# Kernel tuning notes

Measured on AMD Instinct MI355X. Metric: run time of the kernel, lower is better.

## Reference

```python
import jax, jax.numpy as jnp
import numpy as np

B, Q, K = 8, 128, 1024
QK_DIM = 512   # query_size == key_size
HID = 256      # hidden_size
VDIM = 512     # value feature dim
NEG = -1e6     # mask fill value used by the torch code


def setup_inputs() -> dict:
    key = jax.random.key(0)
    ks = jax.random.split(key, 7)
    queries = jax.random.normal(ks[0], (B, Q, QK_DIM), dtype=jnp.float32)
    keys = jax.random.normal(ks[1], (B, K, QK_DIM), dtype=jnp.float32)
    values = jax.random.normal(ks[2], (B, K, VDIM), dtype=jnp.float32)
    valid_lens = jax.random.randint(ks[3], (B,), 1, K + 1, dtype=jnp.int32)
    # Linear weights (no bias); scaled like torch default init
    Wq = jax.random.normal(ks[4], (QK_DIM, HID), dtype=jnp.float32) / np.sqrt(QK_DIM)
    Wk = jax.random.normal(ks[5], (QK_DIM, HID), dtype=jnp.float32) / np.sqrt(QK_DIM)
    wv = jax.random.normal(ks[6], (HID,), dtype=jnp.float32) / np.sqrt(HID)
    return {"queries": queries, "keys": keys, "values": values,
            "valid_lens": valid_lens, "Wq": Wq, "Wk": Wk, "wv": wv}


def reference(queries, keys, values, valid_lens, Wq, Wk, wv):
    q = jnp.einsum('bqd,dh->bqh', queries, Wq)          # [B,Q,H]
    k = jnp.einsum('bkd,dh->bkh', keys, Wk)             # [B,K,H]
    # broadcast add -> tanh -> score projection
    features = jnp.tanh(q[:, :, None, :] + k[:, None, :, :])  # [B,Q,K,H]
    scores = jnp.einsum('bqkh,h->bqk', features, wv)    # [B,Q,K]
    # masked softmax over last axis (valid_lens per batch row)
    mask = jnp.arange(scores.shape[-1])[None, None, :] < valid_lens[:, None, None]
    scores = jnp.where(mask, scores, NEG)
    attn = jax.nn.softmax(scores, axis=-1)              # [B,Q,K]
    # dropout is identity in eval mode (p=0)
    return jnp.einsum('bqk,bkv->bqv', attn, values)     # [B,Q,VDIM]
```

## Files before the change

### kernel.cpp

```cpp
#include <hip/hip_runtime.h>
#include <math.h>

#define NB 8
#define NQ 128
#define NK 1024
#define ND 512
#define NH 256
#define NV 512

typedef __attribute__((ext_vector_type(8))) short short8v;
typedef __attribute__((ext_vector_type(4))) float floatx4;


__device__ __forceinline__ ushort f2bf(float f) {
  union { float f; unsigned u; } v; v.f = f;
  unsigned r = (v.u + 0x7FFF + ((v.u >> 16) & 1)) >> 16;
  return (ushort)r;
}
__device__ __forceinline__ float bf2f(ushort b) {
  union { unsigned u; float f; } v; v.u = ((unsigned)b) << 16;
  return v.f;
}
__device__ __forceinline__ float wave_rsum(float v) {
#pragma unroll
  for (int off = 32; off; off >>= 1) v += __shfl_xor(v, off);
  return v;
}

__global__ __launch_bounds__(64) void splitw_kernel(
    const float* __restrict__ Wq, const float* __restrict__ Wk,
    ushort* __restrict__ WpQ, ushort* __restrict__ WpK) {
  const int l = threadIdx.x;
  const int blk = blockIdx.x;
  const float* W = blockIdx.y ? Wk : Wq;
  ushort* O = blockIdx.y ? WpK : WpQ;
  const int col = ((blk >> 4) << 4) + (l & 15);
  const int dbase = (blk & 15) * 32 + ((l >> 4) << 3);
  ushort h8[8], l8[8];
#pragma unroll
  for (int j = 0; j < 8; ++j) {
    float f = W[(size_t)(dbase + j) * NH + col];
    ushort hi = f2bf(f);
    h8[j] = hi;
    l8[j] = f2bf(f - bf2f(hi));
  }
  ushort* oh = &O[(size_t)blk * 1024 + l * 8];
  *(ushort4*)&oh[0] = make_ushort4(h8[0], h8[1], h8[2], h8[3]);
  *(ushort4*)&oh[4] = make_ushort4(h8[4], h8[5], h8[6], h8[7]);
  *(ushort4*)&oh[512] = make_ushort4(l8[0], l8[1], l8[2], l8[3]);
  *(ushort4*)&oh[516] = make_ushort4(l8[4], l8[5], l8[6], l8[7]);
}

__global__ __launch_bounds__(256) void convert_v_kernel(
    const float* __restrict__ values, const int* __restrict__ valid_lens,
    ushort* __restrict__ Vp) {
  const int b = blockIdx.z;
  const int k0 = blockIdx.x * 32;
  const int v0 = blockIdx.y * 32;
  const int V = valid_lens[b];
  if (k0 >= ((V + 31) & ~31)) return;
  const int t = threadIdx.x;
  __shared__ float tile[32][33];
#pragma unroll
  for (int i = 0; i < 4; ++i) {
    int idx = t + 256 * i;
    int kk = idx >> 5, vv = idx & 31;
    tile[kk][vv] = values[(size_t)(b * NK + k0 + kk) * NV + v0 + vv];
  }
  __syncthreads();
  const int vv = t & 31, k4 = t >> 5;
  const int kr = k4 * 4;
  const size_t base = ((size_t)(b * 32 + ((v0 + vv) >> 4)) * 32 + (k0 >> 5)) * 512;
  const int off = ((vv & 15) << 3) + (((kr >> 3) & 3) << 7) + (kr & 7);
  ushort4 o;
  o.x = f2bf(tile[kr + 0][vv]);
  o.y = f2bf(tile[kr + 1][vv]);
  o.z = f2bf(tile[kr + 2][vv]);
  o.w = f2bf(tile[kr + 3][vv]);
  *(ushort4*)&Vp[base + off] = o;
}

__global__ __launch_bounds__(256, 2) void proj_mfma_kernel(
    const float* __restrict__ queries, const float* __restrict__ keys,
    const ushort* __restrict__ WpQ, const ushort* __restrict__ WpK,
    const int* __restrict__ valid_lens,
    float* __restrict__ Eq, ushort* __restrict__ EkTb) {
  const int t = threadIdx.x;
  const int lane = t & 63, wvid = t >> 6;
  const int lr = lane & 15, lg = lane >> 4;
  const int bx = blockIdx.x;
  const bool isQ = bx < 64;
  const float* A;
  const ushort* Wp;
  int arow0, b = 0, rin = 0;
  if (isQ) {
    A = queries; Wp = WpQ; arow0 = bx * 16;
  } else {
    int kt = bx - 64;
    b = kt >> 6; rin = (kt & 63) * 16;
    if (rin >= valid_lens[b]) return;
    A = keys; Wp = WpK; arow0 = b * NK + rin;
  }

  __shared__ ushort Ah[16][520];
  __shared__ ushort Al[16][520];
  {
    const float* Arow = A + (size_t)arow0 * ND;
#pragma unroll
    for (int i = 0; i < 8; ++i) {
      int e = (t + 256 * i) * 4;
      int r = e >> 9, c = e & 511;
      float4 a = *(const float4*)&Arow[e];
      ushort4 h, l;
      h.x = f2bf(a.x); l.x = f2bf(a.x - bf2f(h.x));
      h.y = f2bf(a.y); l.y = f2bf(a.y - bf2f(h.y));
      h.z = f2bf(a.z); l.z = f2bf(a.z - bf2f(h.z));
      h.w = f2bf(a.w); l.w = f2bf(a.w - bf2f(h.w));
      *(ushort4*)&Ah[r][c] = h;
      *(ushort4*)&Al[r][c] = l;
    }
  }
  __syncthreads();

  const ushort* wbase = Wp + (size_t)wvid * 64 * 1024 + lane * 8;

  floatx4 acc[4];
#pragma unroll
  for (int c = 0; c < 4; ++c) acc[c] = (floatx4){0.f, 0.f, 0.f, 0.f};

  short8v wh[3][4], wl[3][4];
  short8v ahb[2], alb[2];

#define LOADW(buf, kkv)                                                    \
  {                                                                        \
    _Pragma("unroll") for (int c = 0; c < 4; ++c) {                        \
      wh[buf][c] = *(const short8v*)&wbase[(size_t)(c * 16 + (kkv)) * 1024];        \
      wl[buf][c] = *(const short8v*)&wbase[(size_t)(c * 16 + (kkv)) * 1024 + 512];  \
    }                                                                      \
  }
#define LOADA(buf, kkv)                                                    \
  {                                                                        \
    ahb[buf] = *(const short8v*)&Ah[lr][(kkv) * 32 + lg * 8];              \
    alb[buf] = *(const short8v*)&Al[lr][(kkv) * 32 + lg * 8];              \
  }

  LOADW(0, 0);
  LOADW(1, 1);
  LOADA(0, 0);
#pragma unroll
  for (int kk = 0; kk < 16; ++kk) {
    if (kk + 2 < 16) LOADW((kk + 2) % 3, kk + 2);
    if (kk + 1 < 16) LOADA((kk + 1) & 1, kk + 1);
    const short8v ah_ = ahb[kk & 1];
    const short8v al_ = alb[kk & 1];
    const int B = kk % 3;
#pragma unroll
    for (int c = 0; c < 4; ++c) {
      acc[c] = __builtin_amdgcn_mfma_f32_16x16x32_bf16(al_, wh[B][c], acc[c], 0, 0, 0);
      acc[c] = __builtin_amdgcn_mfma_f32_16x16x32_bf16(ah_, wl[B][c], acc[c], 0, 0, 0);
      acc[c] = __builtin_amdgcn_mfma_f32_16x16x32_bf16(ah_, wh[B][c], acc[c], 0, 0, 0);
    }
  }
#undef LOADW
#undef LOADA

  const float C2 = 2.885390081777927f;
  if (isQ) {
#pragma unroll
    for (int c = 0; c < 4; ++c) {
      const int h = wvid * 64 + c * 16 + lr;
#pragma unroll
      for (int reg = 0; reg < 4; ++reg) {
        const int row = arow0 + lg * 4 + reg;
        float p = fminf(fmaxf(acc[c][reg], -15.f), 15.f);
        Eq[(size_t)row * NH + h] = exp2f(p * C2);
      }
    }
  } else {
#pragma unroll
    for (int c = 0; c < 4; ++c) {
      const int h = wvid * 64 + c * 16 + lr;
      ushort4 e;
      e.x = f2bf(exp2f(fminf(fmaxf(acc[c][0], -15.f), 15.f) * C2));
      e.y = f2bf(exp2f(fminf(fmaxf(acc[c][1], -15.f), 15.f) * C2));
      e.z = f2bf(exp2f(fminf(fmaxf(acc[c][2], -15.f), 15.f) * C2));
      e.w = f2bf(exp2f(fminf(fmaxf(acc[c][3], -15.f), 15.f) * C2));
      *(ushort4*)&EkTb[((size_t)(b * NH + h)) * NK + rin + lg * 4] = e;
    }
  }
}

__global__ __launch_bounds__(256, 2) void score_kernel(
    const float* __restrict__ Eq, const ushort* __restrict__ EkTb,
    const float* __restrict__ wvp, const int* __restrict__ valid_lens,
    ushort* __restrict__ Pbp, float* __restrict__ rowsum) {
  const int b = blockIdx.z;
  const int V = valid_lens[b];
  const int k0 = blockIdx.y * 256;
  if (k0 >= V) return;
  const int t = threadIdx.x;
  const int q0 = blockIdx.x * 2;
  const int lane = t & 63, wid = t >> 6;
  const float L2E2 = 2.8853900817779268f;

  __shared__ __align__(16) float eqs[2][NH];
  __shared__ __align__(16) float wvs[NH];
  __shared__ float red[8];

  if (t < 128)
    ((float4*)eqs)[t] = ((const float4*)&Eq[(size_t)(b * NQ + q0) * NH])[t];
  wvs[t] = wvp[t];
  __syncthreads();

  float mn = wave_rsum(fminf(wvs[t], 0.f));
  if (lane == 0) red[wid] = mn;
  __syncthreads();
  const float SN = -(red[0] + red[1] + red[2] + red[3]);
  __syncthreads();

  const ushort* ek = EkTb + (size_t)b * NH * NK + k0 + t;
  float acc0 = 0.f, acc1 = 0.f;

  ushort uA[8], uB[8];
#define LOADE(u, h0)                                                      \
  {                                                                       \
    _Pragma("unroll") for (int j = 0; j < 8; ++j)                         \
        u[j] = ek[(size_t)((h0) + j) * NK];                               \
  }
#define CHUNK(u, h0)                                                      \
  {                                                                       \
    float e0[8], e1[8], w8[8];                                            \
    *(float4*)&e0[0] = *(const float4*)&eqs[0][(h0)];                     \
    *(float4*)&e0[4] = *(const float4*)&eqs[0][(h0) + 4];                 \
    *(float4*)&e1[0] = *(const float4*)&eqs[1][(h0)];                     \
    *(float4*)&e1[4] = *(const float4*)&eqs[1][(h0) + 4];                 \
    *(float4*)&w8[0] = *(const float4*)&wvs[(h0)];                        \
    *(float4*)&w8[4] = *(const float4*)&wvs[(h0) + 4];                    \
    _Pragma("unroll") for (int j = 0; j < 8; ++j) {                       \
      const float ev = bf2f(u[j]);                                        \
      acc0 += w8[j] * __builtin_amdgcn_rcpf(__builtin_fmaf(e0[j], ev, 1.f)); \
      acc1 += w8[j] * __builtin_amdgcn_rcpf(__builtin_fmaf(e1[j], ev, 1.f)); \
    }                                                                     \
  }

  LOADE(uA, 0);
#pragma unroll 1
  for (int h0 = 0; h0 < NH; h0 += 16) {
    LOADE(uB, h0 + 8);
    CHUNK(uA, h0);
    if (h0 + 16 < NH) LOADE(uA, h0 + 16);
    CHUNK(uB, h0 + 8);
  }
#undef LOADE
#undef CHUNK

  const int k = k0 + t;
  const float p0 = (k < V) ? exp2f(-L2E2 * (acc0 + SN)) : 0.f;
  const float p1 = (k < V) ? exp2f(-L2E2 * (acc1 + SN)) : 0.f;
  const ushort u0 = f2bf(p0), u1 = f2bf(p1);

  {
    const size_t blk0 = ((size_t)(b * 8 + (q0 >> 4)) * 32 + (k0 >> 5) + (t >> 5)) * 512;
    const int offk = (((t >> 3) & 3) << 7) + (t & 7);
    Pbp[blk0 + ((q0 & 15) << 3) + offk] = u0;
    Pbp[blk0 + (((q0 + 1) & 15) << 3) + offk] = u1;
  }

  float s0 = wave_rsum(bf2f(u0));
  float s1 = wave_rsum(bf2f(u1));
  if (lane == 0) { red[wid] = s0; red[4 + wid] = s1; }
  __syncthreads();
  if (t == 0) {
    atomicAdd(&rowsum[b * NQ + q0], red[0] + red[1] + red[2] + red[3]);
    atomicAdd(&rowsum[b * NQ + q0 + 1], red[4] + red[5] + red[6] + red[7]);
  }
}

__global__ __launch_bounds__(128, 2) void pv_mfma_kernel(
    const ushort* __restrict__ Pbp, const ushort* __restrict__ Vp,
    const float* __restrict__ rowsum, const int* __restrict__ valid_lens,
    float* __restrict__ out) {
  const int w = threadIdx.x >> 6;
  const int lane = threadIdx.x & 63;
  const int lr = lane & 15, lg = lane >> 4;
  const int qt = blockIdx.x, vt2 = blockIdx.y, b = blockIdx.z;
  const int V = valid_lens[b];
  const int Kt4 = (((V + 31) >> 5) + 3) & ~3;
  const int vt = vt2 * 2 + w;
  const ushort* pbase = Pbp + ((size_t)(b * 8 + qt) * 32) * 512 + lane * 8;
  const ushort* vbase = Vp + ((size_t)(b * 32 + vt) * 32) * 512 + lane * 8;

#define LP(s) (*(const short8v*)&pbase[(size_t)(s) * 512])
#define LV(s) (*(const short8v*)&vbase[(size_t)(s) * 512])

  floatx4 acc0 = (floatx4){0.f, 0.f, 0.f, 0.f};
  floatx4 acc1 = (floatx4){0.f, 0.f, 0.f, 0.f};
  short8v pA, vA, pB, vB, pC, vC, pD, vD;
  pA = LP(0); vA = LV(0);
  pB = LP(1); vB = LV(1);
  pC = LP(2); vC = LV(2);
  for (int s = 0; s < Kt4; s += 4) {
    pD = LP(s + 3); vD = LV(s + 3);
    acc0 = __builtin_amdgcn_mfma_f32_16x16x32_bf16(pA, vA, acc0, 0, 0, 0);
    if (s + 4 < Kt4) { pA = LP(s + 4); vA = LV(s + 4); }
    acc1 = __builtin_amdgcn_mfma_f32_16x16x32_bf16(pB, vB, acc1, 0, 0, 0);
    if (s + 5 < Kt4) { pB = LP(s + 5); vB = LV(s + 5); }
    acc0 = __builtin_amdgcn_mfma_f32_16x16x32_bf16(pC, vC, acc0, 0, 0, 0);
    if (s + 6 < Kt4) { pC = LP(s + 6); vC = LV(s + 6); }
    acc1 = __builtin_amdgcn_mfma_f32_16x16x32_bf16(pD, vD, acc1, 0, 0, 0);
  }
#undef LP
#undef LV

#pragma unroll
  for (int reg = 0; reg < 4; ++reg) {
    const int row = b * NQ + qt * 16 + lg * 4 + reg;
    const float rs = __builtin_amdgcn_rcpf(rowsum[row]);
    out[(size_t)row * NV + vt * 16 + lr] = (acc0[reg] + acc1[reg]) * rs;
  }
}

extern "C" void kernel_launch(void* const* d_in, const int* in_sizes, int n_in,
                              void* d_out, int out_size, void* d_ws, size_t ws_size,
                              hipStream_t stream) {
  const float* queries = (const float*)d_in[0];
  const float* keys    = (const float*)d_in[1];
  const float* values  = (const float*)d_in[2];
  const int*   vlens   = (const int*)d_in[3];
  const float* Wq      = (const float*)d_in[4];
  const float* Wk      = (const float*)d_in[5];
  const float* wv      = (const float*)d_in[6];
  float* out = (float*)d_out;

  char* base = (char*)d_ws;
  ushort* WpQ  = (ushort*)base;
  ushort* WpK  = WpQ + 256 * 1024;
  float*  Eq   = (float*)(base + (1 << 20));
  ushort* EkTb = (ushort*)(base + (2 << 20));
  ushort* Pbp  = (ushort*)(base + (6 << 20));
  ushort* Vp   = (ushort*)(base + (8 << 20));
  float*  rowsum = (float*)(base + (16 << 20));

  hipMemsetAsync(rowsum, 0, NB * NQ * sizeof(float), stream);
  splitw_kernel<<<dim3(256, 2), dim3(64), 0, stream>>>(Wq, Wk, WpQ, WpK);
  convert_v_kernel<<<dim3(32, 16, 8), dim3(256), 0, stream>>>(values, vlens, Vp);
  proj_mfma_kernel<<<dim3(576), dim3(256), 0, stream>>>(
      queries, keys, WpQ, WpK, vlens, Eq, EkTb);
  score_kernel<<<dim3(64, 4, 8), dim3(256), 0, stream>>>(
      Eq, EkTb, wv, vlens, Pbp, rowsum);
  pv_mfma_kernel<<<dim3(8, 16, 8), dim3(128), 0, stream>>>(
      Pbp, Vp, rowsum, vlens, out);
}
```

Measured before the change: 153.8 us.

## Stage weights via direct global-to-LDS loads, widen score tiles, fold memset

The projection kernel now streams its bf16 weight tiles with global_load_lds into a triple-buffered shared array and synchronises with explicit vmcnt waits. This replaces register prefetch and is meant to cut VGPR pressure and hide load latency, but the large LDS footprint lowers occupancy to one block per CU. The score kernel handles four query rows per block instead of two, so each loaded EkT element serves more queries and the grid halves. The rowsum memset is folded into splitw_kernel to remove one launch.

```diff
diff --git a/kernel.cpp b/kernel.cpp
--- a/kernel.cpp
+++ b/kernel.cpp
@@ -29,9 +29,11 @@
 
 __global__ __launch_bounds__(64) void splitw_kernel(
     const float* __restrict__ Wq, const float* __restrict__ Wk,
-    ushort* __restrict__ WpQ, ushort* __restrict__ WpK) {
+    ushort* __restrict__ WpQ, ushort* __restrict__ WpK,
+    float* __restrict__ rowsum) {
   const int l = threadIdx.x;
   const int blk = blockIdx.x;
+  if (blockIdx.y == 0 && blk < 16) rowsum[blk * 64 + l] = 0.f;
   const float* W = blockIdx.y ? Wk : Wq;
   ushort* O = blockIdx.y ? WpK : WpQ;
   const int col = ((blk >> 4) << 4) + (l & 15);
@@ -80,7 +82,7 @@
   *(ushort4*)&Vp[base + off] = o;
 }
 
-__global__ __launch_bounds__(256, 2) void proj_mfma_kernel(
+__global__ __launch_bounds__(256, 1) void proj_mfma_kernel(
     const float* __restrict__ queries, const float* __restrict__ keys,
     const ushort* __restrict__ WpQ, const ushort* __restrict__ WpK,
     const int* __restrict__ valid_lens,
@@ -102,8 +104,25 @@
     A = keys; Wp = WpK; arow0 = b * NK + rin;
   }
 
+  __shared__ ushort Wlds[3][4][8][512];
   __shared__ ushort Ah[16][520];
   __shared__ ushort Al[16][520];
+
+#define ISSUE(buf, kkv)                                                        \
+  {                                                                            \
+    _Pragma("unroll") for (int f = 0; f < 8; ++f) {                            \
+      const ushort* g = &Wp[((size_t)((wvid * 4 + (f >> 1)) * 16 + (kkv))      \
+                             << 10) + ((f & 1) << 9) + lane * 8];              \
+      __builtin_amdgcn_global_load_lds(                                        \
+          (const __attribute__((address_space(1))) void*)g,                    \
+          (__attribute__((address_space(3))) void*)&Wlds[buf][wvid][f][0],     \
+          16, 0, 0);                                                           \
+    }                                                                          \
+  }
+
+  ISSUE(0, 0);
+  ISSUE(1, 1);
+
   {
     const float* Arow = A + (size_t)arow0 * ND;
 #pragma unroll
@@ -122,47 +141,28 @@
   }
   __syncthreads();
 
-  const ushort* wbase = Wp + (size_t)wvid * 64 * 1024 + lane * 8;
-
   floatx4 acc[4];
 #pragma unroll
   for (int c = 0; c < 4; ++c) acc[c] = (floatx4){0.f, 0.f, 0.f, 0.f};
 
-  short8v wh[3][4], wl[3][4];
-  short8v ahb[2], alb[2];
-
-#define LOADW(buf, kkv)                                                    \
-  {                                                                        \
-    _Pragma("unroll") for (int c = 0; c < 4; ++c) {                        \
-      wh[buf][c] = *(const short8v*)&wbase[(size_t)(c * 16 + (kkv)) * 1024];        \
-      wl[buf][c] = *(const short8v*)&wbase[(size_t)(c * 16 + (kkv)) * 1024 + 512];  \
-    }                                                                      \
-  }
-#define LOADA(buf, kkv)                                                    \
-  {                                                                        \
-    ahb[buf] = *(const short8v*)&Ah[lr][(kkv) * 32 + lg * 8];              \
-    alb[buf] = *(const short8v*)&Al[lr][(kkv) * 32 + lg * 8];              \
-  }
-
-  LOADW(0, 0);
-  LOADW(1, 1);
-  LOADA(0, 0);
 #pragma unroll
   for (int kk = 0; kk < 16; ++kk) {
-    if (kk + 2 < 16) LOADW((kk + 2) % 3, kk + 2);
-    if (kk + 1 < 16) LOADA((kk + 1) & 1, kk + 1);
-    const short8v ah_ = ahb[kk & 1];
-    const short8v al_ = alb[kk & 1];
-    const int B = kk % 3;
+    if (kk + 2 < 16) ISSUE((kk + 2) % 3, kk + 2);
+    if (kk < 14)      asm volatile("s_waitcnt vmcnt(16)" ::: "memory");
+    else if (kk == 14) asm volatile("s_waitcnt vmcnt(8)" ::: "memory");
+    else               asm volatile("s_waitcnt vmcnt(0)" ::: "memory");
+    const short8v ah_ = *(const short8v*)&Ah[lr][kk * 32 + lg * 8];
+    const short8v al_ = *(const short8v*)&Al[lr][kk * 32 + lg * 8];
 #pragma unroll
     for (int c = 0; c < 4; ++c) {
-      acc[c] = __builtin_amdgcn_mfma_f32_16x16x32_bf16(al_, wh[B][c], acc[c], 0, 0, 0);
-      acc[c] = __builtin_amdgcn_mfma_f32_16x16x32_bf16(ah_, wl[B][c], acc[c], 0, 0, 0);
-      acc[c] = __builtin_amdgcn_mfma_f32_16x16x32_bf16(ah_, wh[B][c], acc[c], 0, 0, 0);
+      const short8v wh_ = *(const short8v*)&Wlds[kk % 3][wvid][c * 2 + 0][lane * 8];
+      const short8v wl_ = *(const short8v*)&Wlds[kk % 3][wvid][c * 2 + 1][lane * 8];
+      acc[c] = __builtin_amdgcn_mfma_f32_16x16x32_bf16(al_, wh_, acc[c], 0, 0, 0);
+      acc[c] = __builtin_amdgcn_mfma_f32_16x16x32_bf16(ah_, wl_, acc[c], 0, 0, 0);
+      acc[c] = __builtin_amdgcn_mfma_f32_16x16x32_bf16(ah_, wh_, acc[c], 0, 0, 0);
     }
   }
-#undef LOADW
-#undef LOADA
+#undef ISSUE
 
   const float C2 = 2.885390081777927f;
   if (isQ) {
@@ -199,16 +199,15 @@
   const int k0 = blockIdx.y * 256;
   if (k0 >= V) return;
   const int t = threadIdx.x;
-  const int q0 = blockIdx.x * 2;
+  const int q0 = blockIdx.x * 4;
   const int lane = t & 63, wid = t >> 6;
   const float L2E2 = 2.8853900817779268f;
 
-  __shared__ __align__(16) float eqs[2][NH];
+  __shared__ __align__(16) float eqs[4][NH];
   __shared__ __align__(16) float wvs[NH];
-  __shared__ float red[8];
-
-  if (t < 128)
-    ((float4*)eqs)[t] = ((const float4*)&Eq[(size_t)(b * NQ + q0) * NH])[t];
+  __shared__ float red[20];
+
+  ((float4*)eqs)[t] = ((const float4*)&Eq[(size_t)(b * NQ + q0) * NH])[t];
   wvs[t] = wvp[t];
   __syncthreads();
 
@@ -216,10 +215,9 @@
   if (lane == 0) red[wid] = mn;
   __syncthreads();
   const float SN = -(red[0] + red[1] + red[2] + red[3]);
-  __syncthreads();
 
   const ushort* ek = EkTb + (size_t)b * NH * NK + k0 + t;
-  float acc0 = 0.f, acc1 = 0.f;
+  float a0 = 0.f, a1 = 0.f, a2 = 0.f, a3 = 0.f;
 
   ushort uA[8], uB[8];
 #define LOADE(u, h0)                                                      \
@@ -229,17 +227,23 @@
   }
 #define CHUNK(u, h0)                                                      \
   {                                                                       \
-    float e0[8], e1[8], w8[8];                                            \
+    float e0[8], e1[8], e2[8], e3[8], w8[8];                              \
     *(float4*)&e0[0] = *(const float4*)&eqs[0][(h0)];                     \
     *(float4*)&e0[4] = *(const float4*)&eqs[0][(h0) + 4];                 \
     *(float4*)&e1[0] = *(const float4*)&eqs[1][(h0)];                     \
     *(float4*)&e1[4] = *(const float4*)&eqs[1][(h0) + 4];                 \
+    *(float4*)&e2[0] = *(const float4*)&eqs[2][(h0)];                     \
+    *(float4*)&e2[4] = *(const float4*)&eqs[2][(h0) + 4];                 \
+    *(float4*)&e3[0] = *(const float4*)&eqs[3][(h0)];                     \
+    *(float4*)&e3[4] = *(const float4*)&eqs[3][(h0) + 4];                 \
     *(float4*)&w8[0] = *(const float4*)&wvs[(h0)];                        \
     *(float4*)&w8[4] = *(const float4*)&wvs[(h0) + 4];                    \
     _Pragma("unroll") for (int j = 0; j < 8; ++j) {                       \
       const float ev = bf2f(u[j]);                                        \
-      acc0 += w8[j] * __builtin_amdgcn_rcpf(__builtin_fmaf(e0[j], ev, 1.f)); \
-      acc1 += w8[j] * __builtin_amdgcn_rcpf(__builtin_fmaf(e1[j], ev, 1.f)); \
+      a0 += w8[j] * __builtin_amdgcn_rcpf(__builtin_fmaf(e0[j], ev, 1.f)); \
+      a1 += w8[j] * __builtin_amdgcn_rcpf(__builtin_fmaf(e1[j], ev, 1.f)); \
+      a2 += w8[j] * __builtin_amdgcn_rcpf(__builtin_fmaf(e2[j], ev, 1.f)); \
+      a3 += w8[j] * __builtin_amdgcn_rcpf(__builtin_fmaf(e3[j], ev, 1.f)); \
     }                                                                     \
   }
 
@@ -255,25 +259,26 @@
 #undef CHUNK
 
   const int k = k0 + t;
-  const float p0 = (k < V) ? exp2f(-L2E2 * (acc0 + SN)) : 0.f;
-  const float p1 = (k < V) ? exp2f(-L2E2 * (acc1 + SN)) : 0.f;
-  const ushort u0 = f2bf(p0), u1 = f2bf(p1);
-
-  {
-    const size_t blk0 = ((size_t)(b * 8 + (q0 >> 4)) * 32 + (k0 >> 5) + (t >> 5)) * 512;
-    const int offk = (((t >> 3) & 3) << 7) + (t & 7);
-    Pbp[blk0 + ((q0 & 15) << 3) + offk] = u0;
-    Pbp[blk0 + (((q0 + 1) & 15) << 3) + offk] = u1;
-  }
-
-  float s0 = wave_rsum(bf2f(u0));
-  float s1 = wave_rsum(bf2f(u1));
-  if (lane == 0) { red[wid] = s0; red[4 + wid] = s1; }
-  __syncthreads();
-  if (t == 0) {
-    atomicAdd(&rowsum[b * NQ + q0], red[0] + red[1] + red[2] + red[3]);
-    atomicAdd(&rowsum[b * NQ + q0 + 1], red[4] + red[5] + red[6] + red[7]);
-  }
+  const bool ok = (k < V);
+  float p[4];
+  p[0] = ok ? exp2f(-L2E2 * (a0 + SN)) : 0.f;
+  p[1] = ok ? exp2f(-L2E2 * (a1 + SN)) : 0.f;
+  p[2] = ok ? exp2f(-L2E2 * (a2 + SN)) : 0.f;
+  p[3] = ok ? exp2f(-L2E2 * (a3 + SN)) : 0.f;
+
+  const size_t blk0 = ((size_t)(b * 8 + (q0 >> 4)) * 32 + (k0 >> 5) + (t >> 5)) * 512;
+  const int offk = (((t >> 3) & 3) << 7) + (t & 7);
+#pragma unroll
+  for (int i = 0; i < 4; ++i) {
+    const ushort ui = f2bf(p[i]);
+    Pbp[blk0 + (((q0 + i) & 15) << 3) + offk] = ui;
+    float s = wave_rsum(bf2f(ui));
+    if (lane == 0) red[4 + i * 4 + wid] = s;
+  }
+  __syncthreads();
+  if (t < 4)
+    atomicAdd(&rowsum[b * NQ + q0 + t],
+              red[4 + t * 4] + red[5 + t * 4] + red[6 + t * 4] + red[7 + t * 4]);
 }
 
 __global__ __launch_bounds__(128, 2) void pv_mfma_kernel(
@@ -341,12 +346,11 @@
   ushort* Vp   = (ushort*)(base + (8 << 20));
   float*  rowsum = (float*)(base + (16 << 20));
 
-  hipMemsetAsync(rowsum, 0, NB * NQ * sizeof(float), stream);
-  splitw_kernel<<<dim3(256, 2), dim3(64), 0, stream>>>(Wq, Wk, WpQ, WpK);
+  splitw_kernel<<<dim3(256, 2), dim3(64), 0, stream>>>(Wq, Wk, WpQ, WpK, rowsum);
   convert_v_kernel<<<dim3(32, 16, 8), dim3(256), 0, stream>>>(values, vlens, Vp);
   proj_mfma_kernel<<<dim3(576), dim3(256), 0, stream>>>(
       queries, keys, WpQ, WpK, vlens, Eq, EkTb);
-  score_kernel<<<dim3(64, 4, 8), dim3(256), 0, stream>>>(
+  score_kernel<<<dim3(32, 4, 8), dim3(256), 0, stream>>>(
       Eq, EkTb, wv, vlens, Pbp, rowsum);
   pv_mfma_kernel<<<dim3(8, 16, 8), dim3(128), 0, stream>>>(
       Pbp, Vp, rowsum, vlens, out);
```

Result: faster. 150.5 us (-2.1%).
